# Optimization experiments

Hardware: AMD Instinct MI355X
Metric: run time of the kernel (lower is better)

The kernel has to match this reference:

```python
import jax, jax.numpy as jnp
import numpy as np

IN_FF = 7  # joints
MASK = np.ones(9, dtype=np.float32)  # [P(3), RPY sin/cos (6)]


def _mlp(x, params):
    # params: list of (W, b); sigmoid after every layer except the last (predict)
    h = x
    for W, b in params[:-1]:
        h = jax.nn.sigmoid(h @ W + b)
    W, b = params[-1]
    return h @ W + b


def _rpy_head(x, params):
    # FeedForwardNet_RPY forward: y -> [sin(y0), cos(y1)], angle = atan2(sin, cos)
    y = _mlp(x, params)
    s = jnp.sin(y[..., 0])
    c = jnp.cos(y[..., 1])
    ang = jnp.arctan2(s, c)
    return jnp.stack([s, c, ang], axis=-1)  # (..., 3)


def setup_inputs():
    key = jax.random.key(0)
    ks = jax.random.split(key, 26)
    m = 16384
    d = {"x": jax.random.normal(ks[0], (m, 2 * IN_FF), jnp.float32)}

    def lin(k, fi, fo, name, i):
        k1, k2 = jax.random.split(k)
        lim = 1.0 / np.sqrt(fi)  # torch Linear default init
        d[name + "_W" + str(i)] = jax.random.uniform(k1, (fi, fo), jnp.float32, -lim, lim)
        d[name + "_b" + str(i)] = jax.random.uniform(k2, (fo,), jnp.float32, -lim, lim)

    idx = 1
    for name, dims in [("pos", [7, 512, 512, 3]), ("roll", [7, 256, 256, 2]),
                       ("pitch", [7, 256, 256, 2]), ("yaw", [7, 256, 256, 2])]:
        for i in range(3):
            lin(ks[idx], dims[i], dims[i + 1], name, i)
            idx += 1
    return d


def _forward(x, pos_p, roll_p, pitch_p, yaw_p):
    mask = jnp.asarray(MASK)
    M_P, M_RPY = mask[:3], mask[3:]
    q, qdot = x[:, :IN_FF], x[:, IN_FF:]

    # position net: forward + per-sample Jacobian (exact, replaces the autograd loop)
    P = _mlp(q, pos_p)                                          # (m, 3)
    J_P = jax.vmap(jax.jacfwd(lambda z: _mlp(z, pos_p)))(q)     # (m, 3, 7)
    vel = jnp.einsum("moi,mi->mo", J_P, qdot)                   # bmm(J_P, jointVels)
    P = P * M_P
    vel = vel * M_P

    heads = []
    for p in (roll_p, pitch_p, yaw_p):
        f = lambda z, p=p: _rpy_head(z, p)
        y = f(q)                                # (m, 3): [sin, cos, angle]
        J = jax.vmap(jax.jacfwd(f))(q)          # (m, 3, 7)
        v = jnp.einsum("moi,mi->mo", J[:, :2, :], qdot)  # (m, 2)
        heads.append((y, J, v))
    (yR, JR, vR), (yPi, JPi, vPi), (yY, JY, vY) = heads

    # order: [roll_sin, pitch_sin, yaw_sin, roll_cos, pitch_cos, yaw_cos]
    RPY = jnp.stack([yR[:, 0], yPi[:, 0], yY[:, 0], yR[:, 1], yPi[:, 1], yY[:, 1]], axis=1) * M_RPY
    vel_RPY = jnp.stack([vR[:, 0], vPi[:, 0], vY[:, 0], vR[:, 1], vPi[:, 1], vY[:, 1]], axis=1) * M_RPY
    J_RPY = jnp.stack([JR[:, 0], JPi[:, 0], JY[:, 0], JR[:, 1], JPi[:, 1], JY[:, 1]], axis=1)  # (m,6,7)

    out = jnp.concatenate([P, RPY, vel, vel_RPY], axis=1)            # (m, 18)
    J_tot = jnp.concatenate([J_P, J_RPY], axis=1)                    # (m, 9, 7)
    out_angles = jnp.concatenate([P, yR[:, 2:3], yPi[:, 2:3], yY[:, 2:3]], axis=1)       # (m, 6)
    J_tot_angles = jnp.concatenate([J_P, JR[:, 2:3], JPi[:, 2:3], JY[:, 2:3]], axis=1)   # (m, 6, 7)
    return out, J_tot, out_angles, J_tot_angles


def reference(x, pos_W0, pos_b0, pos_W1, pos_b1, pos_W2, pos_b2,
              roll_W0, roll_b0, roll_W1, roll_b1, roll_W2, roll_b2,
              pitch_W0, pitch_b0, pitch_W1, pitch_b1, pitch_W2, pitch_b2,
              yaw_W0, yaw_b0, yaw_W1, yaw_b1, yaw_W2, yaw_b2):
    pos_p = [(pos_W0, pos_b0), (pos_W1, pos_b1), (pos_W2, pos_b2)]
    roll_p = [(roll_W0, roll_b0), (roll_W1, roll_b1), (roll_W2, roll_b2)]
    pitch_p = [(pitch_W0, pitch_b0), (pitch_W1, pitch_b1), (pitch_W2, pitch_b2)]
    yaw_p = [(yaw_W0, yaw_b0), (yaw_W1, yaw_b1), (yaw_W2, yaw_b2)]
    return _forward(x, pos_p, roll_p, pitch_p, yaw_p)
```

## Files before the change

kernel.cpp:

```cpp
#include <hip/hip_runtime.h>
#include <math.h>

typedef __attribute__((ext_vector_type(8))) short short8;
typedef __attribute__((ext_vector_type(4))) float floatx4;

__device__ __forceinline__ float sig(float z) { return 1.0f / (1.0f + __expf(-z)); }

__device__ __forceinline__ unsigned short f2bf(float f) {
    unsigned u = __float_as_uint(f);
    u = (u + 0x7FFFu + ((u >> 16) & 1u)) >> 16;
    return (unsigned short)u;
}

__global__ void convert_w1(const float* __restrict__ src, unsigned short* __restrict__ dst,
                           int H, int logH) {
    int idx = blockIdx.x * 256 + threadIdx.x;
    if (idx >= H * H) return;
    int n = idx & (H - 1), k = idx >> logH;
    int KT = H >> 5;
    int blk = (n >> 4) * KT + (k >> 5);
    int lane = ((k >> 3) & 3) * 16 + (n & 15);
    int j = k & 7;
    dst[(blk * 64 + lane) * 8 + j] = f2bf(src[idx]);
}

__global__ __launch_bounds__(256, 2)
void pos_mfma(const float* __restrict__ x,
              const float* __restrict__ W0, const float* __restrict__ b0,
              const float* __restrict__ b1,
              const float* __restrict__ W2, const float* __restrict__ b2,
              const unsigned short* __restrict__ wsW1,
              float* __restrict__ out, int ns)
{
    extern __shared__ unsigned short sA[];
    __shared__ float sB0[512];
    __shared__ float sB1[512];
    __shared__ float sW2[1536];
    __shared__ float sQ[8][8];
    __shared__ float sQd[8][8];
    __shared__ float sAcc[2][64][3];
    __shared__ float sSum[64][3];

    const int tid = threadIdx.x;
    const int m0  = blockIdx.x * 8;

    for (int i = tid; i < 512;  i += 256) { sB0[i] = b0[i]; sB1[i] = b1[i]; }
    for (int i = tid; i < 1536; i += 256) sW2[i] = W2[i];
    if (tid < 112) {
        int m = tid / 14, c = tid % 14;
        float v = x[(m0 + m) * 14 + c];
        if (c < 7) sQ[m][c] = v; else sQd[m][c - 7] = v;
    }
    __syncthreads();

    const float4* W04 = (const float4*)W0;
    #pragma unroll
    for (int t = 0; t < 2; ++t) {
        int item = tid + t * 256;
        int s = item >> 6, k8 = item & 63;
        float q[7], w0v[7][8];
        #pragma unroll
        for (int i = 0; i < 7; i++) {
            q[i] = sQ[s][i];
            float4 a = W04[i * 128 + k8 * 2], b4 = W04[i * 128 + k8 * 2 + 1];
            w0v[i][0]=a.x; w0v[i][1]=a.y; w0v[i][2]=a.z; w0v[i][3]=a.w;
            w0v[i][4]=b4.x; w0v[i][5]=b4.y; w0v[i][6]=b4.z; w0v[i][7]=b4.w;
        }
        float hv[8], dv[8];
        #pragma unroll
        for (int jj = 0; jj < 8; jj++) {
            float z = sB0[k8 * 8 + jj];
            #pragma unroll
            for (int i = 0; i < 7; i++) z = fmaf(q[i], w0v[i][jj], z);
            float h = sig(z);
            hv[jj] = h; dv[jj] = h - h * h;
        }
        int kt = k8 >> 2, kq = k8 & 3, sw = kt & 7;
        int rr0 = s * 8;
        {
            short8 v;
            #pragma unroll
            for (int jj = 0; jj < 8; jj++) v[jj] = (short)f2bf(hv[jj]);
            *(short8*)&sA[((rr0 >> 4) * 16 + kt) * 512 + ((kq * 16 + (rr0 & 15)) ^ sw) * 8] = v;
        }
        #pragma unroll
        for (int i = 0; i < 7; i++) {
            int rr = rr0 + 1 + i;
            short8 v;
            #pragma unroll
            for (int jj = 0; jj < 8; jj++) v[jj] = (short)f2bf(dv[jj] * w0v[i][jj]);
            *(short8*)&sA[((rr >> 4) * 16 + kt) * 512 + ((kq * 16 + (rr & 15)) ^ sw) * 8] = v;
        }
    }
    __syncthreads();

    const int w = tid >> 6, lane = tid & 63;
    const int rta = (w & 1) * 2, nh = w >> 1;
    const int quad = lane >> 4, col = lane & 15;
    const int srcl = lane & 47;
    const floatx4 z4 = {0.f, 0.f, 0.f, 0.f};

    floatx4 acc[2][16];
    #pragma unroll
    for (int rt = 0; rt < 2; rt++)
        #pragma unroll
        for (int ct = 0; ct < 16; ct++) acc[rt][ct] = z4;

    for (int kt = 0; kt < 16; ++kt) {
        const int sw = kt & 7;
        short8 bf[16];
        const short8* bp = (const short8*)wsW1 + (size_t)(nh * 16 * 16 + kt) * 64 + lane;
        #pragma unroll
        for (int ct = 0; ct < 16; ++ct) bf[ct] = bp[ct * 16 * 64];
        short8 a0 = *(const short8*)&sA[((rta + 0) * 16 + kt) * 512 + (lane ^ sw) * 8];
        short8 a1 = *(const short8*)&sA[((rta + 1) * 16 + kt) * 512 + (lane ^ sw) * 8];
        #pragma unroll
        for (int ct = 0; ct < 16; ++ct) {
            acc[0][ct] = __builtin_amdgcn_mfma_f32_16x16x32_bf16(a0, bf[ct], acc[0][ct], 0, 0, 0);
            acc[1][ct] = __builtin_amdgcn_mfma_f32_16x16x32_bf16(a1, bf[ct], acc[1][ct], 0, 0, 0);
        }
    }

    float ep[2][4][3];
    #pragma unroll
    for (int a = 0; a < 2; a++) for (int b = 0; b < 4; b++) for (int c = 0; c < 3; c++) ep[a][b][c] = 0.f;

    #pragma unroll
    for (int ct = 0; ct < 16; ++ct) {
        const int n = nh * 256 + ct * 16 + col;
        const float b1n = sB1[n];
        const float w20 = sW2[n * 3], w21 = sW2[n * 3 + 1], w22 = sW2[n * 3 + 2];
        #pragma unroll
        for (int rt2 = 0; rt2 < 2; ++rt2) {
            float z2c = __shfl(acc[rt2][ct][0], srcl);
            float h2 = sig(z2c + b1n);
            float d2 = h2 - h2 * h2;
            #pragma unroll
            for (int r = 0; r < 4; ++r) {
                float g = ((quad & 1) == 0 && r == 0) ? h2 : d2 * acc[rt2][ct][r];
                ep[rt2][r][0] = fmaf(g, w20, ep[rt2][r][0]);
                ep[rt2][r][1] = fmaf(g, w21, ep[rt2][r][1]);
                ep[rt2][r][2] = fmaf(g, w22, ep[rt2][r][2]);
            }
        }
    }

    #pragma unroll
    for (int mask = 1; mask <= 8; mask <<= 1)
        #pragma unroll
        for (int a = 0; a < 2; a++)
            #pragma unroll
            for (int b = 0; b < 4; b++)
                #pragma unroll
                for (int c = 0; c < 3; c++)
                    ep[a][b][c] += __shfl_xor(ep[a][b][c], mask);
    if (col == 0) {
        #pragma unroll
        for (int rt2 = 0; rt2 < 2; ++rt2)
            #pragma unroll
            for (int r = 0; r < 4; ++r) {
                int row = (rta + rt2) * 16 + quad * 4 + r;
                sAcc[nh][row][0] = ep[rt2][r][0];
                sAcc[nh][row][1] = ep[rt2][r][1];
                sAcc[nh][row][2] = ep[rt2][r][2];
            }
    }
    __syncthreads();

    const long JTOT = (long)ns * 18, OUTA = (long)ns * 81, JANG = (long)ns * 87;
    if (tid < 192) {
        int row = tid / 3, j = tid % 3;
        float v = sAcc[0][row][j] + sAcc[1][row][j];
        int s = row >> 3, i = row & 7;
        long M = m0 + s;
        if (i == 0) { v += b2[j]; out[M * 18 + j] = v; out[OUTA + M * 6 + j] = v; }
        else        { out[JTOT + M * 63 + j * 7 + (i - 1)] = v;
                      out[JANG + M * 42 + j * 7 + (i - 1)] = v; }
        sSum[row][j] = v;
    }
    __syncthreads();
    if (tid < 24) {
        int s = tid / 3, j = tid % 3;
        float vel = 0.f;
        #pragma unroll
        for (int i = 0; i < 7; i++) vel = fmaf(sSum[s * 8 + 1 + i][j], sQd[s][i], vel);
        out[(long)(m0 + s) * 18 + 9 + j] = vel;
    }
}

__global__ __launch_bounds__(256, 2)
void rpy_mfma(const float* __restrict__ x,
              const float* __restrict__ rW0, const float* __restrict__ rb0,
              const float* __restrict__ rb1,
              const float* __restrict__ rW2, const float* __restrict__ rb2,
              const float* __restrict__ pW0, const float* __restrict__ pb0,
              const float* __restrict__ pb1,
              const float* __restrict__ pW2, const float* __restrict__ pb2,
              const float* __restrict__ yW0, const float* __restrict__ yb0,
              const float* __restrict__ yb1,
              const float* __restrict__ yW2, const float* __restrict__ yb2,
              const unsigned short* __restrict__ wsBase,
              float* __restrict__ out, int ns)
{
    extern __shared__ unsigned short sA[];
    __shared__ float sB0[256];
    __shared__ float sB1[256];
    __shared__ float sW2[512];
    __shared__ float sQ[16][8];
    __shared__ float sQd[16][8];
    __shared__ float sAcc[2][128][2];
    __shared__ float sSum[128][2];

    const int tid = threadIdx.x;
    const int m0  = blockIdx.x * 16;
    const int h   = blockIdx.y;

    const float* W0 = (h == 0) ? rW0 : (h == 1) ? pW0 : yW0;
    const float* b0 = (h == 0) ? rb0 : (h == 1) ? pb0 : yb0;
    const float* b1 = (h == 0) ? rb1 : (h == 1) ? pb1 : yb1;
    const float* W2 = (h == 0) ? rW2 : (h == 1) ? pW2 : yW2;
    const float* b2 = (h == 0) ? rb2 : (h == 1) ? pb2 : yb2;
    const unsigned short* wsW1 = wsBase + 262144 + h * 65536;

    if (tid < 256) { sB0[tid] = b0[tid]; sB1[tid] = b1[tid]; }
    for (int i = tid; i < 512; i += 256) sW2[i] = W2[i];
    if (tid < 224) {
        int m = tid / 14, c = tid % 14;
        float v = x[(m0 + m) * 14 + c];
        if (c < 7) sQ[m][c] = v; else sQd[m][c - 7] = v;
    }
    __syncthreads();

    const float4* W04 = (const float4*)W0;
    #pragma unroll
    for (int t = 0; t < 2; ++t) {
        int item = tid + t * 256;
        int s = item >> 5, k8 = item & 31;
        float q[7], w0v[7][8];
        #pragma unroll
        for (int i = 0; i < 7; i++) {
            q[i] = sQ[s][i];
            float4 a = W04[i * 64 + k8 * 2], b4 = W04[i * 64 + k8 * 2 + 1];
            w0v[i][0]=a.x; w0v[i][1]=a.y; w0v[i][2]=a.z; w0v[i][3]=a.w;
            w0v[i][4]=b4.x; w0v[i][5]=b4.y; w0v[i][6]=b4.z; w0v[i][7]=b4.w;
        }
        float hv[8], dv[8];
        #pragma unroll
        for (int jj = 0; jj < 8; jj++) {
            float z = sB0[k8 * 8 + jj];
            #pragma unroll
            for (int i = 0; i < 7; i++) z = fmaf(q[i], w0v[i][jj], z);
            float hh = sig(z);
            hv[jj] = hh; dv[jj] = hh - hh * hh;
        }
        int kt = k8 >> 2, kq = k8 & 3, sw = kt & 7;
        int rr0 = s * 8;
        {
            short8 v;
            #pragma unroll
            for (int jj = 0; jj < 8; jj++) v[jj] = (short)f2bf(hv[jj]);
            *(short8*)&sA[((rr0 >> 4) * 8 + kt) * 512 + ((kq * 16 + (rr0 & 15)) ^ sw) * 8] = v;
        }
        #pragma unroll
        for (int i = 0; i < 7; i++) {
            int rr = rr0 + 1 + i;
            short8 v;
            #pragma unroll
            for (int jj = 0; jj < 8; jj++) v[jj] = (short)f2bf(dv[jj] * w0v[i][jj]);
            *(short8*)&sA[((rr >> 4) * 8 + kt) * 512 + ((kq * 16 + (rr & 15)) ^ sw) * 8] = v;
        }
    }
    __syncthreads();

    const int w = tid >> 6, lane = tid & 63;
    const int rta = (w & 1) * 4, nh = w >> 1;
    const int quad = lane >> 4, col = lane & 15;
    const int srcl = lane & 47;
    const floatx4 z4 = {0.f, 0.f, 0.f, 0.f};

    floatx4 acc[4][8];
    #pragma unroll
    for (int rt = 0; rt < 4; rt++)
        #pragma unroll
        for (int ct = 0; ct < 8; ct++) acc[rt][ct] = z4;

    for (int kt = 0; kt < 8; ++kt) {
        const int sw = kt & 7;
        short8 bf[8];
        const short8* bp = (const short8*)wsW1 + (size_t)(nh * 8 * 8 + kt) * 64 + lane;
        #pragma unroll
        for (int ct = 0; ct < 8; ++ct) bf[ct] = bp[ct * 8 * 64];
        short8 a[4];
        #pragma unroll
        for (int rt = 0; rt < 4; ++rt)
            a[rt] = *(const short8*)&sA[((rta + rt) * 8 + kt) * 512 + (lane ^ sw) * 8];
        #pragma unroll
        for (int ct = 0; ct < 8; ++ct)
            #pragma unroll
            for (int rt = 0; rt < 4; ++rt)
                acc[rt][ct] = __builtin_amdgcn_mfma_f32_16x16x32_bf16(a[rt], bf[ct], acc[rt][ct], 0, 0, 0);
    }

    float ep[4][4][2];
    #pragma unroll
    for (int a = 0; a < 4; a++) for (int b = 0; b < 4; b++) for (int c = 0; c < 2; c++) ep[a][b][c] = 0.f;

    #pragma unroll
    for (int ct = 0; ct < 8; ++ct) {
        const int n = nh * 128 + ct * 16 + col;
        const float b1n = sB1[n];
        const float w20 = sW2[n * 2], w21 = sW2[n * 2 + 1];
        #pragma unroll
        for (int rt2 = 0; rt2 < 4; ++rt2) {
            float z2c = __shfl(acc[rt2][ct][0], srcl);
            float h2 = sig(z2c + b1n);
            float d2 = h2 - h2 * h2;
            #pragma unroll
            for (int r = 0; r < 4; ++r) {
                float g = ((quad & 1) == 0 && r == 0) ? h2 : d2 * acc[rt2][ct][r];
                ep[rt2][r][0] = fmaf(g, w20, ep[rt2][r][0]);
                ep[rt2][r][1] = fmaf(g, w21, ep[rt2][r][1]);
            }
        }
    }

    #pragma unroll
    for (int mask = 1; mask <= 8; mask <<= 1)
        #pragma unroll
        for (int a = 0; a < 4; a++)
            #pragma unroll
            for (int b = 0; b < 4; b++)
                #pragma unroll
                for (int c = 0; c < 2; c++)
                    ep[a][b][c] += __shfl_xor(ep[a][b][c], mask);
    if (col == 0) {
        #pragma unroll
        for (int rt2 = 0; rt2 < 4; ++rt2)
            #pragma unroll
            for (int r = 0; r < 4; ++r) {
                int row = (rta + rt2) * 16 + quad * 4 + r;
                sAcc[nh][row][0] = ep[rt2][r][0];
                sAcc[nh][row][1] = ep[rt2][r][1];
            }
    }
    __syncthreads();

    if (tid < 256) {
        int row = tid >> 1, j = tid & 1;
        float v = sAcc[0][row][j] + sAcc[1][row][j];
        if ((row & 7) == 0) v += b2[j];
        sSum[row][j] = v;
    }
    __syncthreads();

    const long JTOT = (long)ns * 18, OUTA = (long)ns * 81, JANG = (long)ns * 87;
    if (tid < 16) {
        int s = tid;
        long M = m0 + s;
        float y0 = sSum[s * 8][0], y1 = sSum[s * 8][1];
        float sv = sinf(y0), cv = cosf(y1);
        out[M * 18 + 3 + h] = sv;
        out[M * 18 + 6 + h] = cv;
        out[OUTA + M * 6 + 3 + h] = atan2f(sv, cv);
        float f0 = cosf(y0), f1 = -sinf(y1);
        float inv = 1.0f / fmaf(sv, sv, cv * cv);
        float v0 = 0.f, v1 = 0.f;
        #pragma unroll
        for (int i = 0; i < 7; i++) {
            float r0 = f0 * sSum[s * 8 + 1 + i][0];
            float r1 = f1 * sSum[s * 8 + 1 + i][1];
            out[JTOT + M * 63 + (3 + h) * 7 + i] = r0;
            out[JTOT + M * 63 + (6 + h) * 7 + i] = r1;
            out[JANG + M * 42 + (3 + h) * 7 + i] = (cv * r0 - sv * r1) * inv;
            v0 = fmaf(r0, sQd[s][i], v0);
            v1 = fmaf(r1, sQd[s][i], v1);
        }
        out[M * 18 + 12 + h] = v0;
        out[M * 18 + 15 + h] = v1;
    }
}

extern "C" void kernel_launch(void* const* d_in, const int* in_sizes, int n_in,
                              void* d_out, int out_size, void* d_ws, size_t ws_size,
                              hipStream_t stream) {
    (void)n_in; (void)out_size; (void)ws_size;
    const float* x = (const float*)d_in[0];
    float* out = (float*)d_out;
    unsigned short* ws = (unsigned short*)d_ws;
    const int ns = in_sizes[0] / 14;

    convert_w1<<<dim3((512 * 512) / 256), 256, 0, stream>>>((const float*)d_in[3],  ws,          512, 9);
    convert_w1<<<dim3((256 * 256) / 256), 256, 0, stream>>>((const float*)d_in[9],  ws + 262144, 256, 8);
    convert_w1<<<dim3((256 * 256) / 256), 256, 0, stream>>>((const float*)d_in[15], ws + 327680, 256, 8);
    convert_w1<<<dim3((256 * 256) / 256), 256, 0, stream>>>((const float*)d_in[21], ws + 393216, 256, 8);

    pos_mfma<<<dim3(ns / 8), 256, 65536, stream>>>(
        x,
        (const float*)d_in[1], (const float*)d_in[2],
        (const float*)d_in[4],
        (const float*)d_in[5], (const float*)d_in[6],
        ws, out, ns);

    rpy_mfma<<<dim3(ns / 16, 3), 256, 65536, stream>>>(
        x,
        (const float*)d_in[7],  (const float*)d_in[8],  (const float*)d_in[10],
        (const float*)d_in[11], (const float*)d_in[12],
        (const float*)d_in[13], (const float*)d_in[14], (const float*)d_in[16],
        (const float*)d_in[17], (const float*)d_in[18],
        (const float*)d_in[19], (const float*)d_in[20], (const float*)d_in[22],
        (const float*)d_in[23], (const float*)d_in[24],
        ws, out, ns);
}
```

Baseline: 339.5 us.

## Tile both MLP kernels over K and N with LDS-staged W1 and larger row blocks

Each block now handles 32 samples (256 rows) and walks layer 2 in N-panels and K-slices. For each slice it computes the layer-1 activations and Jacobian rows on the fly into LDS and stages the matching bf16 W1 tile into shared memory. Each wave now owns all N columns of its 64 rows, so the cross-wave partial-sum reduction goes away. The aim is to reuse W1 loads across four times as many rows and to shrink dynamic LDS. The cost is recomputing layer 1 once per N-panel and adding two barriers per K-step.

After: 416.2 us. 22.6% more time.

```diff
diff --git a/kernel.cpp b/kernel.cpp
--- a/kernel.cpp
+++ b/kernel.cpp
@@ -2,6 +2,7 @@
 #include <math.h>
 
 typedef __attribute__((ext_vector_type(8))) short short8;
+typedef __attribute__((ext_vector_type(4))) short short4e;
 typedef __attribute__((ext_vector_type(4))) float floatx4;
 
 __device__ __forceinline__ float sig(float z) { return 1.0f / (1.0f + __expf(-z)); }
@@ -32,115 +33,133 @@
               const unsigned short* __restrict__ wsW1,
               float* __restrict__ out, int ns)
 {
-    extern __shared__ unsigned short sA[];
+    extern __shared__ unsigned short sMem[];
+    unsigned short* sA = sMem;
+    unsigned short* sB = sMem + 16384;
     __shared__ float sB0[512];
     __shared__ float sB1[512];
     __shared__ float sW2[1536];
-    __shared__ float sQ[8][8];
-    __shared__ float sQd[8][8];
-    __shared__ float sAcc[2][64][3];
-    __shared__ float sSum[64][3];
+    __shared__ float sQ[32][8];
+    __shared__ float sQd[32][8];
+    __shared__ float sSum[256][3];
 
     const int tid = threadIdx.x;
-    const int m0  = blockIdx.x * 8;
+    const int m0  = blockIdx.x * 32;
 
     for (int i = tid; i < 512;  i += 256) { sB0[i] = b0[i]; sB1[i] = b1[i]; }
     for (int i = tid; i < 1536; i += 256) sW2[i] = W2[i];
-    if (tid < 112) {
-        int m = tid / 14, c = tid % 14;
+    for (int idx = tid; idx < 448; idx += 256) {
+        int m = idx / 14, c = idx % 14;
         float v = x[(m0 + m) * 14 + c];
         if (c < 7) sQ[m][c] = v; else sQd[m][c - 7] = v;
     }
     __syncthreads();
 
-    const float4* W04 = (const float4*)W0;
-    #pragma unroll
-    for (int t = 0; t < 2; ++t) {
-        int item = tid + t * 256;
-        int s = item >> 6, k8 = item & 63;
-        float q[7], w0v[7][8];
-        #pragma unroll
-        for (int i = 0; i < 7; i++) {
-            q[i] = sQ[s][i];
-            float4 a = W04[i * 128 + k8 * 2], b4 = W04[i * 128 + k8 * 2 + 1];
-            w0v[i][0]=a.x; w0v[i][1]=a.y; w0v[i][2]=a.z; w0v[i][3]=a.w;
-            w0v[i][4]=b4.x; w0v[i][5]=b4.y; w0v[i][6]=b4.z; w0v[i][7]=b4.w;
-        }
-        float hv[8], dv[8];
-        #pragma unroll
-        for (int jj = 0; jj < 8; jj++) {
-            float z = sB0[k8 * 8 + jj];
-            #pragma unroll
-            for (int i = 0; i < 7; i++) z = fmaf(q[i], w0v[i][jj], z);
-            float h = sig(z);
-            hv[jj] = h; dv[jj] = h - h * h;
-        }
-        int kt = k8 >> 2, kq = k8 & 3, sw = kt & 7;
-        int rr0 = s * 8;
-        {
-            short8 v;
-            #pragma unroll
-            for (int jj = 0; jj < 8; jj++) v[jj] = (short)f2bf(hv[jj]);
-            *(short8*)&sA[((rr0 >> 4) * 16 + kt) * 512 + ((kq * 16 + (rr0 & 15)) ^ sw) * 8] = v;
-        }
-        #pragma unroll
-        for (int i = 0; i < 7; i++) {
-            int rr = rr0 + 1 + i;
-            short8 v;
-            #pragma unroll
-            for (int jj = 0; jj < 8; jj++) v[jj] = (short)f2bf(dv[jj] * w0v[i][jj]);
-            *(short8*)&sA[((rr >> 4) * 16 + kt) * 512 + ((kq * 16 + (rr & 15)) ^ sw) * 8] = v;
-        }
-    }
-    __syncthreads();
-
     const int w = tid >> 6, lane = tid & 63;
-    const int rta = (w & 1) * 2, nh = w >> 1;
     const int quad = lane >> 4, col = lane & 15;
     const int srcl = lane & 47;
+    const float4* W04 = (const float4*)W0;
     const floatx4 z4 = {0.f, 0.f, 0.f, 0.f};
 
-    floatx4 acc[2][16];
+    float ep[4][4][3];
     #pragma unroll
-    for (int rt = 0; rt < 2; rt++)
-        #pragma unroll
-        for (int ct = 0; ct < 16; ct++) acc[rt][ct] = z4;
-
-    for (int kt = 0; kt < 16; ++kt) {
-        const int sw = kt & 7;
-        short8 bf[16];
-        const short8* bp = (const short8*)wsW1 + (size_t)(nh * 16 * 16 + kt) * 64 + lane;
-        #pragma unroll
-        for (int ct = 0; ct < 16; ++ct) bf[ct] = bp[ct * 16 * 64];
-        short8 a0 = *(const short8*)&sA[((rta + 0) * 16 + kt) * 512 + (lane ^ sw) * 8];
-        short8 a1 = *(const short8*)&sA[((rta + 1) * 16 + kt) * 512 + (lane ^ sw) * 8];
-        #pragma unroll
-        for (int ct = 0; ct < 16; ++ct) {
-            acc[0][ct] = __builtin_amdgcn_mfma_f32_16x16x32_bf16(a0, bf[ct], acc[0][ct], 0, 0, 0);
-            acc[1][ct] = __builtin_amdgcn_mfma_f32_16x16x32_bf16(a1, bf[ct], acc[1][ct], 0, 0, 0);
+    for (int a = 0; a < 4; a++) for (int b = 0; b < 4; b++) for (int c = 0; c < 3; c++) ep[a][b][c] = 0.f;
+
+    for (int np = 0; np < 4; ++np) {
+        floatx4 acc[4][8];
+        #pragma unroll
+        for (int rt = 0; rt < 4; rt++)
+            #pragma unroll
+            for (int ct = 0; ct < 8; ct++) acc[rt][ct] = z4;
+
+        for (int kt = 0; kt < 8; ++kt) {
+            #pragma unroll
+            for (int it = 0; it < 2; ++it) {
+                int idx = tid + it * 256;
+                int s = idx >> 4, g = idx & 15;
+                int kb = kt * 64 + g * 4;
+                int ks = g >> 3, kq = (g >> 1) & 3, j0 = (g & 1) * 4;
+                int f = kq | (ks << 2);
+                float q[7]; float4 w0r[7];
+                #pragma unroll
+                for (int i = 0; i < 7; i++) { q[i] = sQ[s][i]; w0r[i] = W04[i * 128 + (kb >> 2)]; }
+                float hv[4], dv[4];
+                #pragma unroll
+                for (int jj = 0; jj < 4; jj++) {
+                    float z = sB0[kb + jj];
+                    #pragma unroll
+                    for (int i = 0; i < 7; i++) z = fmaf(q[i], ((const float*)&w0r[i])[jj], z);
+                    float hh = sig(z);
+                    hv[jj] = hh; dv[jj] = hh - hh * hh;
+                }
+                int r0 = s * 8;
+                {
+                    int rtg = r0 >> 4, r15 = r0 & 15;
+                    int a16 = (rtg * 2 + ks) * 64 + kq * 16 + (r15 ^ f);
+                    short4e v;
+                    #pragma unroll
+                    for (int jj = 0; jj < 4; jj++) v[jj] = (short)f2bf(hv[jj]);
+                    *(short4e*)&sA[a16 * 8 + j0] = v;
+                }
+                #pragma unroll
+                for (int i = 0; i < 7; i++) {
+                    int rr = r0 + 1 + i;
+                    int rtg = rr >> 4, r15 = rr & 15;
+                    int a16 = (rtg * 2 + ks) * 64 + kq * 16 + (r15 ^ f);
+                    short4e v;
+                    #pragma unroll
+                    for (int jj = 0; jj < 4; jj++) v[jj] = (short)f2bf(dv[jj] * ((const float*)&w0r[i])[jj]);
+                    *(short4e*)&sA[a16 * 8 + j0] = v;
+                }
+            }
+            #pragma unroll
+            for (int p = 0; p < 4; ++p) {
+                int idx = tid + p * 256;
+                int ct = idx >> 7, ks = (idx >> 6) & 1, ll = idx & 63;
+                size_t blk = (size_t)((np * 8 + ct) * 16 + kt * 2 + ks);
+                short8 v = *(const short8*)(wsW1 + (blk * 64 + ll) * 8);
+                *(short8*)&sB[((ct * 2 + ks) * 64 + ll) * 8] = v;
+            }
+            __syncthreads();
+            short8 afr[4][2];
+            #pragma unroll
+            for (int rt = 0; rt < 4; ++rt) {
+                int rtg = w * 4 + rt;
+                #pragma unroll
+                for (int ks = 0; ks < 2; ++ks) {
+                    int a16 = (rtg * 2 + ks) * 64 + quad * 16 + (col ^ (quad | (ks << 2)));
+                    afr[rt][ks] = *(const short8*)&sA[a16 * 8];
+                }
+            }
+            #pragma unroll
+            for (int ct = 0; ct < 8; ++ct) {
+                short8 bf0 = *(const short8*)&sB[((ct * 2 + 0) * 64 + lane) * 8];
+                short8 bf1 = *(const short8*)&sB[((ct * 2 + 1) * 64 + lane) * 8];
+                #pragma unroll
+                for (int rt = 0; rt < 4; ++rt) {
+                    acc[rt][ct] = __builtin_amdgcn_mfma_f32_16x16x32_bf16(afr[rt][0], bf0, acc[rt][ct], 0, 0, 0);
+                    acc[rt][ct] = __builtin_amdgcn_mfma_f32_16x16x32_bf16(afr[rt][1], bf1, acc[rt][ct], 0, 0, 0);
+                }
+            }
+            __syncthreads();
         }
-    }
-
-    float ep[2][4][3];
-    #pragma unroll
-    for (int a = 0; a < 2; a++) for (int b = 0; b < 4; b++) for (int c = 0; c < 3; c++) ep[a][b][c] = 0.f;
-
-    #pragma unroll
-    for (int ct = 0; ct < 16; ++ct) {
-        const int n = nh * 256 + ct * 16 + col;
-        const float b1n = sB1[n];
-        const float w20 = sW2[n * 3], w21 = sW2[n * 3 + 1], w22 = sW2[n * 3 + 2];
-        #pragma unroll
-        for (int rt2 = 0; rt2 < 2; ++rt2) {
-            float z2c = __shfl(acc[rt2][ct][0], srcl);
-            float h2 = sig(z2c + b1n);
-            float d2 = h2 - h2 * h2;
-            #pragma unroll
-            for (int r = 0; r < 4; ++r) {
-                float g = ((quad & 1) == 0 && r == 0) ? h2 : d2 * acc[rt2][ct][r];
-                ep[rt2][r][0] = fmaf(g, w20, ep[rt2][r][0]);
-                ep[rt2][r][1] = fmaf(g, w21, ep[rt2][r][1]);
-                ep[rt2][r][2] = fmaf(g, w22, ep[rt2][r][2]);
+        #pragma unroll
+        for (int ct = 0; ct < 8; ++ct) {
+            const int n = np * 128 + ct * 16 + col;
+            const float b1n = sB1[n];
+            const float w20 = sW2[n * 3], w21 = sW2[n * 3 + 1], w22 = sW2[n * 3 + 2];
+            #pragma unroll
+            for (int rt = 0; rt < 4; ++rt) {
+                float z2c = __shfl(acc[rt][ct][0], srcl);
+                float h2 = sig(z2c + b1n);
+                float d2 = h2 - h2 * h2;
+                #pragma unroll
+                for (int r = 0; r < 4; ++r) {
+                    float g2 = ((quad & 1) == 0 && r == 0) ? h2 : d2 * acc[rt][ct][r];
+                    ep[rt][r][0] = fmaf(g2, w20, ep[rt][r][0]);
+                    ep[rt][r][1] = fmaf(g2, w21, ep[rt][r][1]);
+                    ep[rt][r][2] = fmaf(g2, w22, ep[rt][r][2]);
+                }
             }
         }
     }
@@ -148,7 +167,7 @@
     #pragma unroll
     for (int mask = 1; mask <= 8; mask <<= 1)
         #pragma unroll
-        for (int a = 0; a < 2; a++)
+        for (int a = 0; a < 4; a++)
             #pragma unroll
             for (int b = 0; b < 4; b++)
                 #pragma unroll
@@ -156,35 +175,33 @@
                     ep[a][b][c] += __shfl_xor(ep[a][b][c], mask);
     if (col == 0) {
         #pragma unroll
-        for (int rt2 = 0; rt2 < 2; ++rt2)
+        for (int rt = 0; rt < 4; ++rt)
             #pragma unroll
             for (int r = 0; r < 4; ++r) {
-                int row = (rta + rt2) * 16 + quad * 4 + r;
-                sAcc[nh][row][0] = ep[rt2][r][0];
-                sAcc[nh][row][1] = ep[rt2][r][1];
-                sAcc[nh][row][2] = ep[rt2][r][2];
+                int row = w * 64 + rt * 16 + quad * 4 + r;
+                sSum[row][0] = ep[rt][r][0];
+                sSum[row][1] = ep[rt][r][1];
+                sSum[row][2] = ep[rt][r][2];
             }
     }
     __syncthreads();
 
-    const long JTOT = (long)ns * 18, OUTA = (long)ns * 81, JANG = (long)ns * 87;
-    if (tid < 192) {
-        int row = tid / 3, j = tid % 3;
-        float v = sAcc[0][row][j] + sAcc[1][row][j];
+    const size_t JTOT = (size_t)ns * 18, OUTA = (size_t)ns * 81, JANG = (size_t)ns * 87;
+    for (int e = tid; e < 768; e += 256) {
+        int row = e / 3, j = e % 3;
+        float v = sSum[row][j];
         int s = row >> 3, i = row & 7;
-        long M = m0 + s;
+        size_t M = m0 + s;
         if (i == 0) { v += b2[j]; out[M * 18 + j] = v; out[OUTA + M * 6 + j] = v; }
         else        { out[JTOT + M * 63 + j * 7 + (i - 1)] = v;
                       out[JANG + M * 42 + j * 7 + (i - 1)] = v; }
-        sSum[row][j] = v;
-    }
-    __syncthreads();
-    if (tid < 24) {
+    }
+    if (tid < 96) {
         int s = tid / 3, j = tid % 3;
         float vel = 0.f;
         #pragma unroll
         for (int i = 0; i < 7; i++) vel = fmaf(sSum[s * 8 + 1 + i][j], sQd[s][i], vel);
-        out[(long)(m0 + s) * 18 + 9 + j] = vel;
+        out[(size_t)(m0 + s) * 18 + 9 + j] = vel;
     }
 }
 
@@ -202,17 +219,18 @@
               const unsigned short* __restrict__ wsBase,
               float* __restrict__ out, int ns)
 {
-    extern __shared__ unsigned short sA[];
+    extern __shared__ unsigned short sMem[];
+    unsigned short* sA = sMem;
+    unsigned short* sB = sMem + 16384;
     __shared__ float sB0[256];
     __shared__ float sB1[256];
     __shared__ float sW2[512];
-    __shared__ float sQ[16][8];
-    __shared__ float sQd[16][8];
-    __shared__ float sAcc[2][128][2];
-    __shared__ float sSum[128][2];
+    __shared__ float sQ[32][8];
+    __shared__ float sQd[32][8];
+    __shared__ float sSum[256][2];
 
     const int tid = threadIdx.x;
-    const int m0  = blockIdx.x * 16;
+    const int m0  = blockIdx.x * 32;
     const int h   = blockIdx.y;
 
     const float* W0 = (h == 0) ? rW0 : (h == 1) ? pW0 : yW0;
@@ -224,102 +242,117 @@
 
     if (tid < 256) { sB0[tid] = b0[tid]; sB1[tid] = b1[tid]; }
     for (int i = tid; i < 512; i += 256) sW2[i] = W2[i];
-    if (tid < 224) {
-        int m = tid / 14, c = tid % 14;
+    for (int idx = tid; idx < 448; idx += 256) {
+        int m = idx / 14, c = idx % 14;
         float v = x[(m0 + m) * 14 + c];
         if (c < 7) sQ[m][c] = v; else sQd[m][c - 7] = v;
     }
     __syncthreads();
 
-    const float4* W04 = (const float4*)W0;
-    #pragma unroll
-    for (int t = 0; t < 2; ++t) {
-        int item = tid + t * 256;
-        int s = item >> 5, k8 = item & 31;
-        float q[7], w0v[7][8];
-        #pragma unroll
-        for (int i = 0; i < 7; i++) {
-            q[i] = sQ[s][i];
-            float4 a = W04[i * 64 + k8 * 2], b4 = W04[i * 64 + k8 * 2 + 1];
-            w0v[i][0]=a.x; w0v[i][1]=a.y; w0v[i][2]=a.z; w0v[i][3]=a.w;
-            w0v[i][4]=b4.x; w0v[i][5]=b4.y; w0v[i][6]=b4.z; w0v[i][7]=b4.w;
-        }
-        float hv[8], dv[8];
-        #pragma unroll
-        for (int jj = 0; jj < 8; jj++) {
-            float z = sB0[k8 * 8 + jj];
-            #pragma unroll
-            for (int i = 0; i < 7; i++) z = fmaf(q[i], w0v[i][jj], z);
-            float hh = sig(z);
-            hv[jj] = hh; dv[jj] = hh - hh * hh;
-        }
-        int kt = k8 >> 2, kq = k8 & 3, sw = kt & 7;
-        int rr0 = s * 8;
-        {
-            short8 v;
-            #pragma unroll
-            for (int jj = 0; jj < 8; jj++) v[jj] = (short)f2bf(hv[jj]);
-            *(short8*)&sA[((rr0 >> 4) * 8 + kt) * 512 + ((kq * 16 + (rr0 & 15)) ^ sw) * 8] = v;
-        }
-        #pragma unroll
-        for (int i = 0; i < 7; i++) {
-            int rr = rr0 + 1 + i;
-            short8 v;
-            #pragma unroll
-            for (int jj = 0; jj < 8; jj++) v[jj] = (short)f2bf(dv[jj] * w0v[i][jj]);
-            *(short8*)&sA[((rr >> 4) * 8 + kt) * 512 + ((kq * 16 + (rr & 15)) ^ sw) * 8] = v;
-        }
-    }
-    __syncthreads();
-
     const int w = tid >> 6, lane = tid & 63;
-    const int rta = (w & 1) * 4, nh = w >> 1;
     const int quad = lane >> 4, col = lane & 15;
     const int srcl = lane & 47;
+    const float4* W04 = (const float4*)W0;
     const floatx4 z4 = {0.f, 0.f, 0.f, 0.f};
-
-    floatx4 acc[4][8];
-    #pragma unroll
-    for (int rt = 0; rt < 4; rt++)
-        #pragma unroll
-        for (int ct = 0; ct < 8; ct++) acc[rt][ct] = z4;
-
-    for (int kt = 0; kt < 8; ++kt) {
-        const int sw = kt & 7;
-        short8 bf[8];
-        const short8* bp = (const short8*)wsW1 + (size_t)(nh * 8 * 8 + kt) * 64 + lane;
-        #pragma unroll
-        for (int ct = 0; ct < 8; ++ct) bf[ct] = bp[ct * 8 * 64];
-        short8 a[4];
-        #pragma unroll
-        for (int rt = 0; rt < 4; ++rt)
-            a[rt] = *(const short8*)&sA[((rta + rt) * 8 + kt) * 512 + (lane ^ sw) * 8];
-        #pragma unroll
-        for (int ct = 0; ct < 8; ++ct)
-            #pragma unroll
-            for (int rt = 0; rt < 4; ++rt)
-                acc[rt][ct] = __builtin_amdgcn_mfma_f32_16x16x32_bf16(a[rt], bf[ct], acc[rt][ct], 0, 0, 0);
-    }
 
     float ep[4][4][2];
     #pragma unroll
     for (int a = 0; a < 4; a++) for (int b = 0; b < 4; b++) for (int c = 0; c < 2; c++) ep[a][b][c] = 0.f;
 
-    #pragma unroll
-    for (int ct = 0; ct < 8; ++ct) {
-        const int n = nh * 128 + ct * 16 + col;
-        const float b1n = sB1[n];
-        const float w20 = sW2[n * 2], w21 = sW2[n * 2 + 1];
-        #pragma unroll
-        for (int rt2 = 0; rt2 < 4; ++rt2) {
-            float z2c = __shfl(acc[rt2][ct][0], srcl);
-            float h2 = sig(z2c + b1n);
-            float d2 = h2 - h2 * h2;
-            #pragma unroll
-            for (int r = 0; r < 4; ++r) {
-                float g = ((quad & 1) == 0 && r == 0) ? h2 : d2 * acc[rt2][ct][r];
-                ep[rt2][r][0] = fmaf(g, w20, ep[rt2][r][0]);
-                ep[rt2][r][1] = fmaf(g, w21, ep[rt2][r][1]);
+    for (int np = 0; np < 2; ++np) {
+        floatx4 acc[4][8];
+        #pragma unroll
+        for (int rt = 0; rt < 4; rt++)
+            #pragma unroll
+            for (int ct = 0; ct < 8; ct++) acc[rt][ct] = z4;
+
+        for (int kt = 0; kt < 4; ++kt) {
+            #pragma unroll
+            for (int it = 0; it < 2; ++it) {
+                int idx = tid + it * 256;
+                int s = idx >> 4, g = idx & 15;
+                int kb = kt * 64 + g * 4;
+                int ks = g >> 3, kq = (g >> 1) & 3, j0 = (g & 1) * 4;
+                int f = kq | (ks << 2);
+                float q[7]; float4 w0r[7];
+                #pragma unroll
+                for (int i = 0; i < 7; i++) { q[i] = sQ[s][i]; w0r[i] = W04[i * 64 + (kb >> 2)]; }
+                float hv[4], dv[4];
+                #pragma unroll
+                for (int jj = 0; jj < 4; jj++) {
+                    float z = sB0[kb + jj];
+                    #pragma unroll
+                    for (int i = 0; i < 7; i++) z = fmaf(q[i], ((const float*)&w0r[i])[jj], z);
+                    float hh = sig(z);
+                    hv[jj] = hh; dv[jj] = hh - hh * hh;
+                }
+                int r0 = s * 8;
+                {
+                    int rtg = r0 >> 4, r15 = r0 & 15;
+                    int a16 = (rtg * 2 + ks) * 64 + kq * 16 + (r15 ^ f);
+                    short4e v;
+                    #pragma unroll
+                    for (int jj = 0; jj < 4; jj++) v[jj] = (short)f2bf(hv[jj]);
+                    *(short4e*)&sA[a16 * 8 + j0] = v;
+                }
+                #pragma unroll
+                for (int i = 0; i < 7; i++) {
+                    int rr = r0 + 1 + i;
+                    int rtg = rr >> 4, r15 = rr & 15;
+                    int a16 = (rtg * 2 + ks) * 64 + kq * 16 + (r15 ^ f);
+                    short4e v;
+                    #pragma unroll
+                    for (int jj = 0; jj < 4; jj++) v[jj] = (short)f2bf(dv[jj] * ((const float*)&w0r[i])[jj]);
+                    *(short4e*)&sA[a16 * 8 + j0] = v;
+                }
+            }
+            #pragma unroll
+            for (int p = 0; p < 4; ++p) {
+                int idx = tid + p * 256;
+                int ct = idx >> 7, ks = (idx >> 6) & 1, ll = idx & 63;
+                size_t blk = (size_t)((np * 8 + ct) * 8 + kt * 2 + ks);
+                short8 v = *(const short8*)(wsW1 + (blk * 64 + ll) * 8);
+                *(short8*)&sB[((ct * 2 + ks) * 64 + ll) * 8] = v;
+            }
+            __syncthreads();
+            short8 afr[4][2];
+            #pragma unroll
+            for (int rt = 0; rt < 4; ++rt) {
+                int rtg = w * 4 + rt;
+                #pragma unroll
+                for (int ks = 0; ks < 2; ++ks) {
+                    int a16 = (rtg * 2 + ks) * 64 + quad * 16 + (col ^ (quad | (ks << 2)));
+                    afr[rt][ks] = *(const short8*)&sA[a16 * 8];
+                }
+            }
+            #pragma unroll
+            for (int ct = 0; ct < 8; ++ct) {
+                short8 bf0 = *(const short8*)&sB[((ct * 2 + 0) * 64 + lane) * 8];
+                short8 bf1 = *(const short8*)&sB[((ct * 2 + 1) * 64 + lane) * 8];
+                #pragma unroll
+                for (int rt = 0; rt < 4; ++rt) {
+                    acc[rt][ct] = __builtin_amdgcn_mfma_f32_16x16x32_bf16(afr[rt][0], bf0, acc[rt][ct], 0, 0, 0);
+                    acc[rt][ct] = __builtin_amdgcn_mfma_f32_16x16x32_bf16(afr[rt][1], bf1, acc[rt][ct], 0, 0, 0);
+                }
+            }
+            __syncthreads();
+        }
+        #pragma unroll
+        for (int ct = 0; ct < 8; ++ct) {
+            const int n = np * 128 + ct * 16 + col;
+            const float b1n = sB1[n];
+            const float w20 = sW2[n * 2], w21 = sW2[n * 2 + 1];
+            #pragma unroll
+            for (int rt = 0; rt < 4; ++rt) {
+                float z2c = __shfl(acc[rt][ct][0], srcl);
+                float h2 = sig(z2c + b1n);
+                float d2 = h2 - h2 * h2;
+                #pragma unroll
+                for (int r = 0; r < 4; ++r) {
+                    float g2 = ((quad & 1) == 0 && r == 0) ? h2 : d2 * acc[rt][ct][r];
+                    ep[rt][r][0] = fmaf(g2, w20, ep[rt][r][0]);
+                    ep[rt][r][1] = fmaf(g2, w21, ep[rt][r][1]);
+                }
             }
         }
     }
@@ -335,29 +368,21 @@
                     ep[a][b][c] += __shfl_xor(ep[a][b][c], mask);
     if (col == 0) {
         #pragma unroll
-        for (int rt2 = 0; rt2 < 4; ++rt2)
+        for (int rt = 0; rt < 4; ++rt)
             #pragma unroll
             for (int r = 0; r < 4; ++r) {
-                int row = (rta + rt2) * 16 + quad * 4 + r;
-                sAcc[nh][row][0] = ep[rt2][r][0];
-                sAcc[nh][row][1] = ep[rt2][r][1];
+                int row = w * 64 + rt * 16 + quad * 4 + r;
+                sSum[row][0] = ep[rt][r][0];
+                sSum[row][1] = ep[rt][r][1];
             }
     }
     __syncthreads();
 
-    if (tid < 256) {
-        int row = tid >> 1, j = tid & 1;
-        float v = sAcc[0][row][j] + sAcc[1][row][j];
-        if ((row & 7) == 0) v += b2[j];
-        sSum[row][j] = v;
-    }
-    __syncthreads();
-
-    const long JTOT = (long)ns * 18, OUTA = (long)ns * 81, JANG = (long)ns * 87;
-    if (tid < 16) {
+    const size_t JTOT = (size_t)ns * 18, OUTA = (size_t)ns * 81, JANG = (size_t)ns * 87;
+    if (tid < 32) {
         int s = tid;
-        long M = m0 + s;
-        float y0 = sSum[s * 8][0], y1 = sSum[s * 8][1];
+        size_t M = m0 + s;
+        float y0 = sSum[s * 8][0] + b2[0], y1 = sSum[s * 8][1] + b2[1];
         float sv = sinf(y0), cv = cosf(y1);
         out[M * 18 + 3 + h] = sv;
         out[M * 18 + 6 + h] = cv;
@@ -394,14 +419,14 @@
     convert_w1<<<dim3((256 * 256) / 256), 256, 0, stream>>>((const float*)d_in[15], ws + 327680, 256, 8);
     convert_w1<<<dim3((256 * 256) / 256), 256, 0, stream>>>((const float*)d_in[21], ws + 393216, 256, 8);
 
-    pos_mfma<<<dim3(ns / 8), 256, 65536, stream>>>(
+    pos_mfma<<<dim3(ns / 32), 256, 49152, stream>>>(
         x,
         (const float*)d_in[1], (const float*)d_in[2],
         (const float*)d_in[4],
         (const float*)d_in[5], (const float*)d_in[6],
         ws, out, ns);
 
-    rpy_mfma<<<dim3(ns / 16, 3), 256, 65536, stream>>>(
+    rpy_mfma<<<dim3(ns / 32, 3), 256, 49152, stream>>>(
         x,
         (const float*)d_in[7],  (const float*)d_in[8],  (const float*)d_in[10],
         (const float*)d_in[11], (const float*)d_in[12],
```

## Split hidden columns across all four waves and double-buffer W1 fragment loads

Applied to the files above, without the earlier changes.

Each wave now covers every row tile and a quarter of the hidden columns, where before the waves were split two ways by rows and two ways by columns. Each wave therefore loads fewer distinct B fragments of W1 from global memory and reuses each one across more row tiles. W1 loads are double-buffered, so the next k-step is fetched while the current MFMAs run, hiding global latency. The cross-wave reduction grows to four partial sums in shared memory, and the extra A fragments and prefetch buffers raise register pressure under the 2-blocks-per-SM launch bound.

After: 338.4 us. No clear change (-0.3%).

```diff
diff --git a/kernel.cpp b/kernel.cpp
--- a/kernel.cpp
+++ b/kernel.cpp
@@ -38,7 +38,7 @@
     __shared__ float sW2[1536];
     __shared__ float sQ[8][8];
     __shared__ float sQd[8][8];
-    __shared__ float sAcc[2][64][3];
+    __shared__ float sAcc[4][64][3];
     __shared__ float sSum[64][3];
 
     const int tid = threadIdx.x;
@@ -95,52 +95,75 @@
     __syncthreads();
 
     const int w = tid >> 6, lane = tid & 63;
-    const int rta = (w & 1) * 2, nh = w >> 1;
     const int quad = lane >> 4, col = lane & 15;
     const int srcl = lane & 47;
     const floatx4 z4 = {0.f, 0.f, 0.f, 0.f};
 
-    floatx4 acc[2][16];
-    #pragma unroll
-    for (int rt = 0; rt < 2; rt++)
-        #pragma unroll
-        for (int ct = 0; ct < 16; ct++) acc[rt][ct] = z4;
-
-    for (int kt = 0; kt < 16; ++kt) {
-        const int sw = kt & 7;
-        short8 bf[16];
-        const short8* bp = (const short8*)wsW1 + (size_t)(nh * 16 * 16 + kt) * 64 + lane;
-        #pragma unroll
-        for (int ct = 0; ct < 16; ++ct) bf[ct] = bp[ct * 16 * 64];
-        short8 a0 = *(const short8*)&sA[((rta + 0) * 16 + kt) * 512 + (lane ^ sw) * 8];
-        short8 a1 = *(const short8*)&sA[((rta + 1) * 16 + kt) * 512 + (lane ^ sw) * 8];
-        #pragma unroll
-        for (int ct = 0; ct < 16; ++ct) {
-            acc[0][ct] = __builtin_amdgcn_mfma_f32_16x16x32_bf16(a0, bf[ct], acc[0][ct], 0, 0, 0);
-            acc[1][ct] = __builtin_amdgcn_mfma_f32_16x16x32_bf16(a1, bf[ct], acc[1][ct], 0, 0, 0);
-        }
-    }
-
-    float ep[2][4][3];
-    #pragma unroll
-    for (int a = 0; a < 2; a++) for (int b = 0; b < 4; b++) for (int c = 0; c < 3; c++) ep[a][b][c] = 0.f;
-
-    #pragma unroll
-    for (int ct = 0; ct < 16; ++ct) {
-        const int n = nh * 256 + ct * 16 + col;
+    floatx4 acc[4][8];
+    #pragma unroll
+    for (int rt = 0; rt < 4; rt++)
+        #pragma unroll
+        for (int ct = 0; ct < 8; ct++) acc[rt][ct] = z4;
+
+    const short8* bbase = (const short8*)wsW1 + (size_t)(w * 8 * 16) * 64 + lane;
+
+    short8 bufA[8], bufB[8];
+    #pragma unroll
+    for (int ct = 0; ct < 8; ++ct) bufA[ct] = bbase[(ct * 16) * 64];
+
+    for (int kt2 = 0; kt2 < 16; kt2 += 2) {
+        #pragma unroll
+        for (int ct = 0; ct < 8; ++ct) bufB[ct] = bbase[(ct * 16 + kt2 + 1) * 64];
+        {
+            const int kt = kt2, sw = kt & 7;
+            short8 afr[4];
+            #pragma unroll
+            for (int rt = 0; rt < 4; ++rt)
+                afr[rt] = *(const short8*)&sA[(rt * 16 + kt) * 512 + (lane ^ sw) * 8];
+            #pragma unroll
+            for (int ct = 0; ct < 8; ++ct)
+                #pragma unroll
+                for (int rt = 0; rt < 4; ++rt)
+                    acc[rt][ct] = __builtin_amdgcn_mfma_f32_16x16x32_bf16(afr[rt], bufA[ct], acc[rt][ct], 0, 0, 0);
+        }
+        if (kt2 + 2 < 16) {
+            #pragma unroll
+            for (int ct = 0; ct < 8; ++ct) bufA[ct] = bbase[(ct * 16 + kt2 + 2) * 64];
+        }
+        {
+            const int kt = kt2 + 1, sw = kt & 7;
+            short8 afr[4];
+            #pragma unroll
+            for (int rt = 0; rt < 4; ++rt)
+                afr[rt] = *(const short8*)&sA[(rt * 16 + kt) * 512 + (lane ^ sw) * 8];
+            #pragma unroll
+            for (int ct = 0; ct < 8; ++ct)
+                #pragma unroll
+                for (int rt = 0; rt < 4; ++rt)
+                    acc[rt][ct] = __builtin_amdgcn_mfma_f32_16x16x32_bf16(afr[rt], bufB[ct], acc[rt][ct], 0, 0, 0);
+        }
+    }
+
+    float ep[4][4][3];
+    #pragma unroll
+    for (int a = 0; a < 4; a++) for (int b = 0; b < 4; b++) for (int c = 0; c < 3; c++) ep[a][b][c] = 0.f;
+
+    #pragma unroll
+    for (int ct = 0; ct < 8; ++ct) {
+        const int n = w * 128 + ct * 16 + col;
         const float b1n = sB1[n];
         const float w20 = sW2[n * 3], w21 = sW2[n * 3 + 1], w22 = sW2[n * 3 + 2];
         #pragma unroll
-        for (int rt2 = 0; rt2 < 2; ++rt2) {
-            float z2c = __shfl(acc[rt2][ct][0], srcl);
+        for (int rt = 0; rt < 4; ++rt) {
+            float z2c = __shfl(acc[rt][ct][0], srcl);
             float h2 = sig(z2c + b1n);
             float d2 = h2 - h2 * h2;
             #pragma unroll
             for (int r = 0; r < 4; ++r) {
-                float g = ((quad & 1) == 0 && r == 0) ? h2 : d2 * acc[rt2][ct][r];
-                ep[rt2][r][0] = fmaf(g, w20, ep[rt2][r][0]);
-                ep[rt2][r][1] = fmaf(g, w21, ep[rt2][r][1]);
-                ep[rt2][r][2] = fmaf(g, w22, ep[rt2][r][2]);
+                float g = ((quad & 1) == 0 && r == 0) ? h2 : d2 * acc[rt][ct][r];
+                ep[rt][r][0] = fmaf(g, w20, ep[rt][r][0]);
+                ep[rt][r][1] = fmaf(g, w21, ep[rt][r][1]);
+                ep[rt][r][2] = fmaf(g, w22, ep[rt][r][2]);
             }
         }
     }
@@ -148,7 +171,7 @@
     #pragma unroll
     for (int mask = 1; mask <= 8; mask <<= 1)
         #pragma unroll
-        for (int a = 0; a < 2; a++)
+        for (int a = 0; a < 4; a++)
             #pragma unroll
             for (int b = 0; b < 4; b++)
                 #pragma unroll
@@ -156,23 +179,23 @@
                     ep[a][b][c] += __shfl_xor(ep[a][b][c], mask);
     if (col == 0) {
         #pragma unroll
-        for (int rt2 = 0; rt2 < 2; ++rt2)
+        for (int rt = 0; rt < 4; ++rt)
             #pragma unroll
             for (int r = 0; r < 4; ++r) {
-                int row = (rta + rt2) * 16 + quad * 4 + r;
-                sAcc[nh][row][0] = ep[rt2][r][0];
-                sAcc[nh][row][1] = ep[rt2][r][1];
-                sAcc[nh][row][2] = ep[rt2][r][2];
+                int row = rt * 16 + quad * 4 + r;
+                sAcc[w][row][0] = ep[rt][r][0];
+                sAcc[w][row][1] = ep[rt][r][1];
+                sAcc[w][row][2] = ep[rt][r][2];
             }
     }
     __syncthreads();
 
-    const long JTOT = (long)ns * 18, OUTA = (long)ns * 81, JANG = (long)ns * 87;
+    const size_t JTOT = (size_t)ns * 18, OUTA = (size_t)ns * 81, JANG = (size_t)ns * 87;
     if (tid < 192) {
         int row = tid / 3, j = tid % 3;
-        float v = sAcc[0][row][j] + sAcc[1][row][j];
+        float v = sAcc[0][row][j] + sAcc[1][row][j] + sAcc[2][row][j] + sAcc[3][row][j];
         int s = row >> 3, i = row & 7;
-        long M = m0 + s;
+        size_t M = m0 + s;
         if (i == 0) { v += b2[j]; out[M * 18 + j] = v; out[OUTA + M * 6 + j] = v; }
         else        { out[JTOT + M * 63 + j * 7 + (i - 1)] = v;
                       out[JANG + M * 42 + j * 7 + (i - 1)] = v; }
@@ -184,7 +207,7 @@
         float vel = 0.f;
         #pragma unroll
         for (int i = 0; i < 7; i++) vel = fmaf(sSum[s * 8 + 1 + i][j], sQd[s][i], vel);
-        out[(long)(m0 + s) * 18 + 9 + j] = vel;
+        out[(size_t)(m0 + s) * 18 + 9 + j] = vel;
     }
 }
 
@@ -208,7 +231,7 @@
     __shared__ float sW2[512];
     __shared__ float sQ[16][8];
     __shared__ float sQd[16][8];
-    __shared__ float sAcc[2][128][2];
+    __shared__ float sAcc[4][128][2];
     __shared__ float sSum[128][2];
 
     const int tid = threadIdx.x;
@@ -273,53 +296,74 @@
     __syncthreads();
 
     const int w = tid >> 6, lane = tid & 63;
-    const int rta = (w & 1) * 4, nh = w >> 1;
     const int quad = lane >> 4, col = lane & 15;
     const int srcl = lane & 47;
     const floatx4 z4 = {0.f, 0.f, 0.f, 0.f};
 
-    floatx4 acc[4][8];
-    #pragma unroll
-    for (int rt = 0; rt < 4; rt++)
-        #pragma unroll
-        for (int ct = 0; ct < 8; ct++) acc[rt][ct] = z4;
-
-    for (int kt = 0; kt < 8; ++kt) {
-        const int sw = kt & 7;
-        short8 bf[8];
-        const short8* bp = (const short8*)wsW1 + (size_t)(nh * 8 * 8 + kt) * 64 + lane;
-        #pragma unroll
-        for (int ct = 0; ct < 8; ++ct) bf[ct] = bp[ct * 8 * 64];
-        short8 a[4];
-        #pragma unroll
-        for (int rt = 0; rt < 4; ++rt)
-            a[rt] = *(const short8*)&sA[((rta + rt) * 8 + kt) * 512 + (lane ^ sw) * 8];
-        #pragma unroll
-        for (int ct = 0; ct < 8; ++ct)
-            #pragma unroll
-            for (int rt = 0; rt < 4; ++rt)
-                acc[rt][ct] = __builtin_amdgcn_mfma_f32_16x16x32_bf16(a[rt], bf[ct], acc[rt][ct], 0, 0, 0);
-    }
-
-    float ep[4][4][2];
-    #pragma unroll
-    for (int a = 0; a < 4; a++) for (int b = 0; b < 4; b++) for (int c = 0; c < 2; c++) ep[a][b][c] = 0.f;
-
-    #pragma unroll
-    for (int ct = 0; ct < 8; ++ct) {
-        const int n = nh * 128 + ct * 16 + col;
+    floatx4 acc[8][4];
+    #pragma unroll
+    for (int rt = 0; rt < 8; rt++)
+        #pragma unroll
+        for (int ct = 0; ct < 4; ct++) acc[rt][ct] = z4;
+
+    const short8* bbase = (const short8*)wsW1 + (size_t)(w * 4 * 8) * 64 + lane;
+
+    short8 bufA[4], bufB[4];
+    #pragma unroll
+    for (int ct = 0; ct < 4; ++ct) bufA[ct] = bbase[(ct * 8) * 64];
+
+    for (int kt2 = 0; kt2 < 8; kt2 += 2) {
+        #pragma unroll
+        for (int ct = 0; ct < 4; ++ct) bufB[ct] = bbase[(ct * 8 + kt2 + 1) * 64];
+        {
+            const int kt = kt2, sw = kt & 7;
+            short8 afr[8];
+            #pragma unroll
+            for (int rt = 0; rt < 8; ++rt)
+                afr[rt] = *(const short8*)&sA[(rt * 8 + kt) * 512 + (lane ^ sw) * 8];
+            #pragma unroll
+            for (int ct = 0; ct < 4; ++ct)
+                #pragma unroll
+                for (int rt = 0; rt < 8; ++rt)
+                    acc[rt][ct] = __builtin_amdgcn_mfma_f32_16x16x32_bf16(afr[rt], bufA[ct], acc[rt][ct], 0, 0, 0);
+        }
+        if (kt2 + 2 < 8) {
+            #pragma unroll
+            for (int ct = 0; ct < 4; ++ct) bufA[ct] = bbase[(ct * 8 + kt2 + 2) * 64];
+        }
+        {
+            const int kt = kt2 + 1, sw = kt & 7;
+            short8 afr[8];
+            #pragma unroll
+            for (int rt = 0; rt < 8; ++rt)
+                afr[rt] = *(const short8*)&sA[(rt * 8 + kt) * 512 + (lane ^ sw) * 8];
+            #pragma unroll
+            for (int ct = 0; ct < 4; ++ct)
+                #pragma unroll
+                for (int rt = 0; rt < 8; ++rt)
+                    acc[rt][ct] = __builtin_amdgcn_mfma_f32_16x16x32_bf16(afr[rt], bufB[ct], acc[rt][ct], 0, 0, 0);
+        }
+    }
+
+    float ep[8][4][2];
+    #pragma unroll
+    for (int a = 0; a < 8; a++) for (int b = 0; b < 4; b++) for (int c = 0; c < 2; c++) ep[a][b][c] = 0.f;
+
+    #pragma unroll
+    for (int ct = 0; ct < 4; ++ct) {
+        const int n = w * 64 + ct * 16 + col;
         const float b1n = sB1[n];
         const float w20 = sW2[n * 2], w21 = sW2[n * 2 + 1];
         #pragma unroll
-        for (int rt2 = 0; rt2 < 4; ++rt2) {
-            float z2c = __shfl(acc[rt2][ct][0], srcl);
+        for (int rt = 0; rt < 8; ++rt) {
+            float z2c = __shfl(acc[rt][ct][0], srcl);
             float h2 = sig(z2c + b1n);
             float d2 = h2 - h2 * h2;
             #pragma unroll
             for (int r = 0; r < 4; ++r) {
-                float g = ((quad & 1) == 0 && r == 0) ? h2 : d2 * acc[rt2][ct][r];
-                ep[rt2][r][0] = fmaf(g, w20, ep[rt2][r][0]);
-                ep[rt2][r][1] = fmaf(g, w21, ep[rt2][r][1]);
+                float g = ((quad & 1) == 0 && r == 0) ? h2 : d2 * acc[rt][ct][r];
+                ep[rt][r][0] = fmaf(g, w20, ep[rt][r][0]);
+                ep[rt][r][1] = fmaf(g, w21, ep[rt][r][1]);
             }
         }
     }
@@ -327,7 +371,7 @@
     #pragma unroll
     for (int mask = 1; mask <= 8; mask <<= 1)
         #pragma unroll
-        for (int a = 0; a < 4; a++)
+        for (int a = 0; a < 8; a++)
             #pragma unroll
             for (int b = 0; b < 4; b++)
                 #pragma unroll
@@ -335,28 +379,28 @@
                     ep[a][b][c] += __shfl_xor(ep[a][b][c], mask);
     if (col == 0) {
         #pragma unroll
-        for (int rt2 = 0; rt2 < 4; ++rt2)
+        for (int rt = 0; rt < 8; ++rt)
             #pragma unroll
             for (int r = 0; r < 4; ++r) {
-                int row = (rta + rt2) * 16 + quad * 4 + r;
-                sAcc[nh][row][0] = ep[rt2][r][0];
-                sAcc[nh][row][1] = ep[rt2][r][1];
+                int row = rt * 16 + quad * 4 + r;
+                sAcc[w][row][0] = ep[rt][r][0];
+                sAcc[w][row][1] = ep[rt][r][1];
             }
     }
     __syncthreads();
 
     if (tid < 256) {
         int row = tid >> 1, j = tid & 1;
-        float v = sAcc[0][row][j] + sAcc[1][row][j];
+        float v = sAcc[0][row][j] + sAcc[1][row][j] + sAcc[2][row][j] + sAcc[3][row][j];
         if ((row & 7) == 0) v += b2[j];
         sSum[row][j] = v;
     }
     __syncthreads();
 
-    const long JTOT = (long)ns * 18, OUTA = (long)ns * 81, JANG = (long)ns * 87;
+    const size_t JTOT = (size_t)ns * 18, OUTA = (size_t)ns * 81, JANG = (size_t)ns * 87;
     if (tid < 16) {
         int s = tid;
-        long M = m0 + s;
+        size_t M = m0 + s;
         float y0 = sSum[s * 8][0], y1 = sSum[s * 8][1];
         float sv = sinf(y0), cv = cosf(y1);
         out[M * 18 + 3 + h] = sv;
```
